# Kernel optimization log

Measured on AMD Instinct MI355X. Metric: run time of the kernel, lower is better.

Reference implementation:

```python
import jax, jax.numpy as jnp
import numpy as np

B, T, D = 16, 2048, 256
WINDOW = 128


def setup_inputs() -> dict:
    key = jax.random.key(0)
    ks = jax.random.split(key, 6)
    scale = 1.0 / np.sqrt(D)
    return {
        "x": jax.random.normal(ks[0], (B, T, D), dtype=jnp.float32),
        "Wq": jax.random.normal(ks[1], (D, D), dtype=jnp.float32) * scale,
        "Wk": jax.random.normal(ks[2], (D, D), dtype=jnp.float32) * scale,
        "Wv": jax.random.normal(ks[3], (D, D), dtype=jnp.float32) * scale,
        "Wo": jax.random.normal(ks[4], (D, D), dtype=jnp.float32) * scale,
        "w_bias": jax.random.normal(ks[5], (T, T), dtype=jnp.float32) * 0.1,
        "window": WINDOW,
    }


def reference(x, Wq, Wk, Wv, Wo, w_bias, window):
    # x: [B,T,D]; w_bias: [T,T] learned pairwise position bias.
    T_ = x.shape[1]
    q = jnp.einsum("btd,de->bte", x, Wq)
    k = jnp.einsum("btd,de->bte", x, Wk)
    v = jnp.einsum("btd,de->bte", x, Wv)

    # AFT-Local: bias is zeroed outside the local band |t - t'| < window,
    # but ALL positions still contribute (with bias 0) to the weighted sum.
    idx = jnp.arange(T_)
    band = jnp.abs(idx[:, None] - idx[None, :]) < window  # [T,T] bool
    w_local = jnp.where(band, w_bias, 0.0)

    # Stable exponentials: the num/den ratio is invariant to per-row shifts
    # of w and per-(b,d) shifts of k.
    w_stable = w_local - jnp.max(w_local, axis=1, keepdims=True)
    k_stable = k - jnp.max(k, axis=1, keepdims=True)
    expw = jnp.exp(w_stable)  # [T,T]
    expk = jnp.exp(k_stable)  # [B,T,D]

    num = jnp.einsum("ts,bsd->btd", expw, expk * v)
    den = jnp.einsum("ts,bsd->btd", expw, expk)
    y = jax.nn.sigmoid(q) * (num / den)
    return jnp.einsum("btd,de->bte", y, Wo)
```

## Files before the change

### kernel.cpp

```cpp
#include <hip/hip_runtime.h>
#include <math.h>

#define B_ 16
#define T_ 2048
#define D_ 256
#define W_ 128
#define M_ (B_*T_)

typedef __attribute__((ext_vector_type(8))) short bf16x8;
typedef __attribute__((ext_vector_type(4))) float f32x4;
typedef unsigned short u16;

static __device__ __forceinline__ u16 f32_bf16_rne(float f) {
    unsigned int u = __float_as_uint(f);
    u += 0x7FFF + ((u >> 16) & 1);
    return (u16)(u >> 16);
}
static __device__ __forceinline__ float bf16_f32(u16 h) {
    return __uint_as_float(((unsigned int)h) << 16);
}

__global__ __launch_bounds__(256) void aft_split_wT(
    const float* __restrict__ Wq, const float* __restrict__ Wk,
    const float* __restrict__ Wv, const float* __restrict__ Wo,
    u16* __restrict__ Wth, u16* __restrict__ Wtl)
{
    const float* Ws[4] = {Wq, Wk, Wv, Wo};
    const float* W = Ws[blockIdx.x];
    const int n  = blockIdx.y * 16 + (threadIdx.x >> 4);
    const int k0 = (threadIdx.x & 15) * 16;
    size_t obase = ((size_t)blockIdx.x * 256 + n) * 256 + k0;
    #pragma unroll 4
    for (int j = 0; j < 16; ++j) {
        float v = W[(size_t)(k0 + j) * 256 + n];
        u16 h = f32_bf16_rne(v);
        Wth[obase + j] = h;
        Wtl[obase + j] = f32_bf16_rne(v - bf16_f32(h));
    }
}

__global__ void aft_ewb(const float* __restrict__ wb, u16* __restrict__ EWb)
{
    const int t = blockIdx.x;
    const int j = threadIdx.x;
    const int s = (t & ~63) - 128 + j;
    const int dlt = s - t;
    float v = 0.f;
    if (s >= 0 && s < T_ && dlt > -W_ && dlt < W_)
        v = expf(wb[(size_t)t * T_ + s]) - 1.0f;
    EWb[(size_t)t * 320 + j] = f32_bf16_rne(v);
}

__global__ __launch_bounds__(256) void aft_qkv_mfma(
    const float* __restrict__ x,
    const u16* __restrict__ Wth, const u16* __restrict__ Wtl,
    u16* __restrict__ ekT, u16* __restrict__ sigqT)
{
    __shared__ alignas(16) u16 sm[25600];
    u16* Ah = sm;
    u16* Al = sm + 5120;
    u16* Bh = sm + 10240;
    u16* Bl = sm + 17920;
    u16* Tr = sm;

    const int tid  = threadIdx.x;
    const int row0 = blockIdx.x * 128;
    const int col0 = blockIdx.y * 64;
    const int b    = row0 >> 11;
    const int t0g  = row0 & (T_ - 1);
    const int lane = tid & 63;
    const int wid  = tid >> 6;
    const int wm   = (wid & 1) * 64;
    const int wn   = (wid >> 1) * 32;
    const int qd   = lane >> 4;
    const int r    = lane & 15;

    f32x4 acc[3][4][2];
    #pragma unroll
    for (int a = 0; a < 3; ++a)
        #pragma unroll
        for (int i = 0; i < 4; ++i)
            #pragma unroll
            for (int j = 0; j < 2; ++j)
                acc[a][i][j] = (f32x4){0.f, 0.f, 0.f, 0.f};

    const int am  = tid >> 1;
    const int akh = (tid & 1) * 16;
    const int bn  = tid >> 2;
    const int bkh = (tid & 3) * 8;

    for (int k0 = 0; k0 < D_; k0 += 32) {
        {
            size_t g = (size_t)(row0 + am) * D_ + k0 + akh;
            #pragma unroll
            for (int c = 0; c < 4; ++c) {
                float4 v = *(const float4*)&x[g + c * 4];
                ushort4 h, l;
                h.x = f32_bf16_rne(v.x); l.x = f32_bf16_rne(v.x - bf16_f32(h.x));
                h.y = f32_bf16_rne(v.y); l.y = f32_bf16_rne(v.y - bf16_f32(h.y));
                h.z = f32_bf16_rne(v.z); l.z = f32_bf16_rne(v.z - bf16_f32(h.z));
                h.w = f32_bf16_rne(v.w); l.w = f32_bf16_rne(v.w - bf16_f32(h.w));
                *(ushort4*)&Ah[am * 40 + akh + c * 4] = h;
                *(ushort4*)&Al[am * 40 + akh + c * 4] = l;
            }
        }
        #pragma unroll
        for (int mat = 0; mat < 3; ++mat) {
            size_t g = ((size_t)mat * 256 + col0 + bn) * 256 + k0 + bkh;
            *(uint4*)&Bh[mat * 2560 + bn * 40 + bkh] = *(const uint4*)&Wth[g];
            *(uint4*)&Bl[mat * 2560 + bn * 40 + bkh] = *(const uint4*)&Wtl[g];
        }
        __syncthreads();

        bf16x8 ah[4], al[4];
        #pragma unroll
        for (int mf = 0; mf < 4; ++mf) {
            ah[mf] = *(const bf16x8*)&Ah[(wm + mf * 16 + r) * 40 + qd * 8];
            al[mf] = *(const bf16x8*)&Al[(wm + mf * 16 + r) * 40 + qd * 8];
        }
        #pragma unroll
        for (int mat = 0; mat < 3; ++mat) {
            #pragma unroll
            for (int nf = 0; nf < 2; ++nf) {
                bf16x8 bh = *(const bf16x8*)&Bh[mat * 2560 + (wn + nf * 16 + r) * 40 + qd * 8];
                bf16x8 bl = *(const bf16x8*)&Bl[mat * 2560 + (wn + nf * 16 + r) * 40 + qd * 8];
                #pragma unroll
                for (int mf = 0; mf < 4; ++mf) {
                    acc[mat][mf][nf] = __builtin_amdgcn_mfma_f32_16x16x32_bf16(ah[mf], bh, acc[mat][mf][nf], 0, 0, 0);
                    acc[mat][mf][nf] = __builtin_amdgcn_mfma_f32_16x16x32_bf16(ah[mf], bl, acc[mat][mf][nf], 0, 0, 0);
                    acc[mat][mf][nf] = __builtin_amdgcn_mfma_f32_16x16x32_bf16(al[mf], bh, acc[mat][mf][nf], 0, 0, 0);
                }
            }
        }
        __syncthreads();
    }

    const int dl_r = tid >> 2;
    const int tseg = (tid & 3) * 32;
    #pragma unroll
    for (int round = 0; round < 3; ++round) {
        __syncthreads();
        #pragma unroll
        for (int mf = 0; mf < 4; ++mf) {
            #pragma unroll
            for (int nf = 0; nf < 2; ++nf) {
                ushort4 o;
                float vals[4];
                #pragma unroll
                for (int reg = 0; reg < 4; ++reg) {
                    float qv = acc[0][mf][nf][reg];
                    float kv = acc[1][mf][nf][reg];
                    float vv = acc[2][mf][nf][reg];
                    if (round == 0)      vals[reg] = expf(kv);
                    else if (round == 1) vals[reg] = expf(kv) * vv;
                    else                 vals[reg] = 1.f / (1.f + expf(-qv));
                }
                o.x = f32_bf16_rne(vals[0]); o.y = f32_bf16_rne(vals[1]);
                o.z = f32_bf16_rne(vals[2]); o.w = f32_bf16_rne(vals[3]);
                int dl = wn + nf * 16 + r;
                int tt = wm + mf * 16 + qd * 4;
                *(ushort4*)&Tr[dl * 136 + tt] = o;
            }
        }
        __syncthreads();
        u16* dst;
        if (round == 0)      dst = ekT   + ((size_t)(b * 512 + col0 + dl_r)) * 2048;
        else if (round == 1) dst = ekT   + ((size_t)(b * 512 + 256 + col0 + dl_r)) * 2048;
        else                 dst = sigqT + ((size_t)(b * 256 + col0 + dl_r)) * 2048;
        dst += t0g + tseg;
        const u16* srcp = &Tr[dl_r * 136 + tseg];
        #pragma unroll
        for (int i = 0; i < 4; ++i)
            *(uint4*)&dst[i * 8] = *(const uint4*)&srcp[i * 8];
    }
}

__global__ __launch_bounds__(256) void aft_sums(
    const u16* __restrict__ ekT, float* __restrict__ Sk, float* __restrict__ Sv)
{
    const int wid  = threadIdx.x >> 6;
    const int lane = threadIdx.x & 63;
    const int row  = blockIdx.x * 4 + wid;
    const int b = row >> 9, n = row & 511;
    const u16* p = ekT + (size_t)row * 2048 + lane * 32;
    float s = 0.f;
    #pragma unroll
    for (int c = 0; c < 4; ++c) {
        union { uint4 v; u16 h[8]; } u;
        u.v = *(const uint4*)&p[c * 8];
        #pragma unroll
        for (int i = 0; i < 8; ++i) s += bf16_f32(u.h[i]);
    }
    #pragma unroll
    for (int off = 32; off >= 1; off >>= 1) s += __shfl_down(s, off, 64);
    if (lane == 0) {
        if (n < 256) Sk[b * 256 + n] = s;
        else         Sv[b * 256 + n - 256] = s;
    }
}

__global__ __launch_bounds__(256) void aft_band_mfma(
    const u16* __restrict__ EWb, const u16* __restrict__ ekT,
    const u16* __restrict__ sigqT,
    const float* __restrict__ Sk, const float* __restrict__ Sv,
    u16* __restrict__ yT)
{
    __shared__ alignas(16) u16 sm[23040];
    u16* Aw  = sm;
    u16* Bkv = sm + 2560;

    const int tid  = threadIdx.x;
    const int t0   = blockIdx.x * 64;
    const int b    = blockIdx.y;
    const int lane = tid & 63;
    const int wid  = tid >> 6;
    const int wn   = wid * 64;
    const int qd   = lane >> 4;
    const int r    = lane & 15;

    f32x4 accn[4][4], accd[4][4];
    #pragma unroll
    for (int i = 0; i < 4; ++i)
        #pragma unroll
        for (int j = 0; j < 4; ++j) {
            accn[i][j] = (f32x4){0.f, 0.f, 0.f, 0.f};
            accd[i][j] = (f32x4){0.f, 0.f, 0.f, 0.f};
        }

    const int atl = tid >> 2;
    const int ak8 = (tid & 3) * 8;

    for (int c = 0; c < 10; ++c) {
        const int sc = t0 - 128 + c * 32;
        if (sc < 0 || sc >= T_) continue;
        __syncthreads();
        *(uint4*)&Aw[atl * 40 + ak8] =
            *(const uint4*)&EWb[(size_t)(t0 + atl) * 320 + c * 32 + ak8];
        #pragma unroll
        for (int rr = 0; rr < 8; ++rr) {
            int n = rr * 64 + atl;
            *(uint4*)&Bkv[n * 40 + ak8] =
                *(const uint4*)&ekT[((size_t)(b * 512) + n) * 2048 + sc + ak8];
        }
        __syncthreads();

        bf16x8 af[4];
        #pragma unroll
        for (int mf = 0; mf < 4; ++mf)
            af[mf] = *(const bf16x8*)&Aw[(mf * 16 + r) * 40 + qd * 8];
        #pragma unroll
        for (int nf = 0; nf < 4; ++nf) {
            bf16x8 be = *(const bf16x8*)&Bkv[(wn + nf * 16 + r) * 40 + qd * 8];
            bf16x8 bv = *(const bf16x8*)&Bkv[(256 + wn + nf * 16 + r) * 40 + qd * 8];
            #pragma unroll
            for (int mf = 0; mf < 4; ++mf) {
                accd[mf][nf] = __builtin_amdgcn_mfma_f32_16x16x32_bf16(af[mf], be, accd[mf][nf], 0, 0, 0);
                accn[mf][nf] = __builtin_amdgcn_mfma_f32_16x16x32_bf16(af[mf], bv, accn[mf][nf], 0, 0, 0);
            }
        }
    }

    #pragma unroll
    for (int nf = 0; nf < 4; ++nf) {
        const int d = wn + nf * 16 + r;
        const float skq = Sk[(b << 8) + d];
        const float svq = Sv[(b << 8) + d];
        #pragma unroll
        for (int mf = 0; mf < 4; ++mf) {
            const int tt = t0 + mf * 16 + qd * 4;
            size_t off = ((size_t)(b << 8) + d) * 2048 + tt;
            ushort4 sg = *(const ushort4*)&sigqT[off];
            ushort4 yo;
            float y0 = bf16_f32(sg.x) * (svq + accn[mf][nf][0]) / (skq + accd[mf][nf][0]);
            float y1 = bf16_f32(sg.y) * (svq + accn[mf][nf][1]) / (skq + accd[mf][nf][1]);
            float y2 = bf16_f32(sg.z) * (svq + accn[mf][nf][2]) / (skq + accd[mf][nf][2]);
            float y3 = bf16_f32(sg.w) * (svq + accn[mf][nf][3]) / (skq + accd[mf][nf][3]);
            yo.x = f32_bf16_rne(y0); yo.y = f32_bf16_rne(y1);
            yo.z = f32_bf16_rne(y2); yo.w = f32_bf16_rne(y3);
            *(ushort4*)&yT[off] = yo;
        }
    }
}

__global__ __launch_bounds__(256) void aft_out_mfma(
    const u16* __restrict__ yT,
    const u16* __restrict__ Woth, const u16* __restrict__ Wotl,
    float* __restrict__ out)
{
    __shared__ alignas(16) u16 sm[15360];
    u16* As = sm;
    u16* Bh = sm + 5120;
    u16* Bl = sm + 10240;

    const int tid  = threadIdx.x;
    const int row0 = blockIdx.x * 128;
    const int col0 = blockIdx.y * 128;
    const int b    = row0 >> 11;
    const int t0g  = row0 & (T_ - 1);
    const int lane = tid & 63;
    const int wid  = tid >> 6;
    const int wm   = (wid & 1) * 64;
    const int wn   = (wid >> 1) * 64;
    const int qd   = lane >> 4;
    const int r    = lane & 15;

    f32x4 acc[4][4];
    #pragma unroll
    for (int i = 0; i < 4; ++i)
        #pragma unroll
        for (int j = 0; j < 4; ++j)
            acc[i][j] = (f32x4){0.f, 0.f, 0.f, 0.f};

    const int dloc = tid & 31;
    const int tb   = (tid >> 5) * 16;
    const int bn   = tid >> 1;
    const int bkh  = (tid & 1) * 16;

    for (int k0 = 0; k0 < D_; k0 += 32) {
        {
            const u16* src = yT + ((size_t)(b * 256) + k0 + dloc) * 2048 + t0g + tb;
            union { uint4 v[2]; u16 h[16]; } u;
            u.v[0] = *(const uint4*)&src[0];
            u.v[1] = *(const uint4*)&src[8];
            #pragma unroll
            for (int i = 0; i < 16; ++i)
                As[(tb + i) * 40 + dloc] = u.h[i];
        }
        {
            size_t g = (size_t)(col0 + bn) * 256 + k0 + bkh;
            *(uint4*)&Bh[bn * 40 + bkh]     = *(const uint4*)&Woth[g];
            *(uint4*)&Bh[bn * 40 + bkh + 8] = *(const uint4*)&Woth[g + 8];
            *(uint4*)&Bl[bn * 40 + bkh]     = *(const uint4*)&Wotl[g];
            *(uint4*)&Bl[bn * 40 + bkh + 8] = *(const uint4*)&Wotl[g + 8];
        }
        __syncthreads();

        bf16x8 af[4];
        #pragma unroll
        for (int mf = 0; mf < 4; ++mf)
            af[mf] = *(const bf16x8*)&As[(wm + mf * 16 + r) * 40 + qd * 8];
        #pragma unroll
        for (int nf = 0; nf < 4; ++nf) {
            bf16x8 bh = *(const bf16x8*)&Bh[(wn + nf * 16 + r) * 40 + qd * 8];
            bf16x8 bl = *(const bf16x8*)&Bl[(wn + nf * 16 + r) * 40 + qd * 8];
            #pragma unroll
            for (int mf = 0; mf < 4; ++mf) {
                acc[mf][nf] = __builtin_amdgcn_mfma_f32_16x16x32_bf16(af[mf], bh, acc[mf][nf], 0, 0, 0);
                acc[mf][nf] = __builtin_amdgcn_mfma_f32_16x16x32_bf16(af[mf], bl, acc[mf][nf], 0, 0, 0);
            }
        }
        __syncthreads();
    }

    #pragma unroll
    for (int mf = 0; mf < 4; ++mf)
        #pragma unroll
        for (int nf = 0; nf < 4; ++nf)
            #pragma unroll
            for (int reg = 0; reg < 4; ++reg) {
                int mrow = row0 + wm + mf * 16 + qd * 4 + reg;
                int ncol = col0 + wn + nf * 16 + r;
                out[(size_t)mrow * D_ + ncol] = acc[mf][nf][reg];
            }
}

extern "C" void kernel_launch(void* const* d_in, const int* in_sizes, int n_in,
                              void* d_out, int out_size, void* d_ws, size_t ws_size,
                              hipStream_t stream)
{
    const float* x  = (const float*)d_in[0];
    const float* Wq = (const float*)d_in[1];
    const float* Wk = (const float*)d_in[2];
    const float* Wv = (const float*)d_in[3];
    const float* Wo = (const float*)d_in[4];
    const float* wb = (const float*)d_in[5];

    u16* Wth   = (u16*)d_ws;
    u16* Wtl   = Wth + 262144;
    u16* EWb   = Wtl + 262144;
    u16* ekT   = EWb + 655360;
    u16* sigqT = ekT + 16777216;
    u16* yT    = sigqT + 8388608;
    float* Sk  = (float*)(yT + 8388608);
    float* Sv  = Sk + 4096;

    aft_split_wT<<<dim3(4, 16), 256, 0, stream>>>(Wq, Wk, Wv, Wo, Wth, Wtl);
    aft_ewb<<<dim3(T_), 320, 0, stream>>>(wb, EWb);
    aft_qkv_mfma<<<dim3(M_ / 128, 4), 256, 0, stream>>>(x, Wth, Wtl, ekT, sigqT);
    aft_sums<<<dim3(8192 / 4), 256, 0, stream>>>(ekT, Sk, Sv);
    aft_band_mfma<<<dim3(T_ / 64, B_), 256, 0, stream>>>(EWb, ekT, sigqT, Sk, Sv, yT);
    aft_out_mfma<<<dim3(M_ / 128, 2), 256, 0, stream>>>(yT, Wth + 3 * 65536, Wtl + 3 * 65536, (float*)d_out);
}
```

Measured before the change: 213.8 us.

## Pre-split x into bf16 hi/lo, use direct global-to-LDS loads, split band/out grids

Adds a separate kernel that splits x into bf16 hi/lo once, so the QKV GEMM can stage A and B tiles with global_load_lds into an XOR-swizzled LDS layout instead of converting in registers. The band kernel is split across two halves of D and the output GEMM uses 64-row tiles, doubling block counts and cutting LDS use per block to raise occupancy. The extra pass writes and rereads x in bf16 hi/lo through memory, which adds an extra kernel launch and global traffic.

```diff
diff --git a/kernel.cpp b/kernel.cpp
--- a/kernel.cpp
+++ b/kernel.cpp
@@ -18,6 +18,11 @@
 }
 static __device__ __forceinline__ float bf16_f32(u16 h) {
     return __uint_as_float(((unsigned int)h) << 16);
+}
+static __device__ __forceinline__ void gload16(const u16* g, u16* lds) {
+    __builtin_amdgcn_global_load_lds(
+        (const __attribute__((address_space(1))) unsigned int*)g,
+        (__attribute__((address_space(3))) unsigned int*)lds, 16, 0, 0);
 }
 
 __global__ __launch_bounds__(256) void aft_split_wT(
@@ -51,16 +56,33 @@
     EWb[(size_t)t * 320 + j] = f32_bf16_rne(v);
 }
 
+__global__ __launch_bounds__(256) void aft_split_x(
+    const float* __restrict__ x, u16* __restrict__ xh, u16* __restrict__ xl)
+{
+    const size_t i0 = ((size_t)blockIdx.x * 256 + threadIdx.x) * 8;
+    float4 v0 = *(const float4*)&x[i0];
+    float4 v1 = *(const float4*)&x[i0 + 4];
+    float v[8] = {v0.x, v0.y, v0.z, v0.w, v1.x, v1.y, v1.z, v1.w};
+    union { uint4 u; u16 h[8]; } H, L;
+    #pragma unroll
+    for (int i = 0; i < 8; ++i) {
+        H.h[i] = f32_bf16_rne(v[i]);
+        L.h[i] = f32_bf16_rne(v[i] - bf16_f32(H.h[i]));
+    }
+    *(uint4*)&xh[i0] = H.u;
+    *(uint4*)&xl[i0] = L.u;
+}
+
 __global__ __launch_bounds__(256) void aft_qkv_mfma(
-    const float* __restrict__ x,
+    const u16* __restrict__ xh, const u16* __restrict__ xl,
     const u16* __restrict__ Wth, const u16* __restrict__ Wtl,
     u16* __restrict__ ekT, u16* __restrict__ sigqT)
 {
-    __shared__ alignas(16) u16 sm[25600];
+    __shared__ alignas(16) u16 sm[20480];
     u16* Ah = sm;
-    u16* Al = sm + 5120;
-    u16* Bh = sm + 10240;
-    u16* Bl = sm + 17920;
+    u16* Al = sm + 4096;
+    u16* Bh = sm + 8192;
+    u16* Bl = sm + 14336;
     u16* Tr = sm;
 
     const int tid  = threadIdx.x;
@@ -74,6 +96,8 @@
     const int wn   = (wid >> 1) * 32;
     const int qd   = lane >> 4;
     const int r    = lane & 15;
+    const int lrow = lane >> 2;
+    const int lseg = lane & 3;
 
     f32x4 acc[3][4][2];
     #pragma unroll
@@ -84,46 +108,43 @@
             for (int j = 0; j < 2; ++j)
                 acc[a][i][j] = (f32x4){0.f, 0.f, 0.f, 0.f};
 
-    const int am  = tid >> 1;
-    const int akh = (tid & 1) * 16;
-    const int bn  = tid >> 2;
-    const int bkh = (tid & 3) * 8;
-
     for (int k0 = 0; k0 < D_; k0 += 32) {
-        {
-            size_t g = (size_t)(row0 + am) * D_ + k0 + akh;
-            #pragma unroll
-            for (int c = 0; c < 4; ++c) {
-                float4 v = *(const float4*)&x[g + c * 4];
-                ushort4 h, l;
-                h.x = f32_bf16_rne(v.x); l.x = f32_bf16_rne(v.x - bf16_f32(h.x));
-                h.y = f32_bf16_rne(v.y); l.y = f32_bf16_rne(v.y - bf16_f32(h.y));
-                h.z = f32_bf16_rne(v.z); l.z = f32_bf16_rne(v.z - bf16_f32(h.z));
-                h.w = f32_bf16_rne(v.w); l.w = f32_bf16_rne(v.w - bf16_f32(h.w));
-                *(ushort4*)&Ah[am * 40 + akh + c * 4] = h;
-                *(ushort4*)&Al[am * 40 + akh + c * 4] = l;
-            }
+        #pragma unroll
+        for (int j = 0; j < 2; ++j) {
+            int rbase = j * 64 + wid * 16;
+            int row   = rbase + lrow;
+            int seg   = lseg ^ ((row >> 1) & 3);
+            size_t g  = (size_t)(row0 + row) * 256 + k0 + seg * 8;
+            gload16(xh + g, &Ah[rbase * 32]);
+            gload16(xl + g, &Al[rbase * 32]);
+        }
+        #pragma unroll
+        for (int m = 0; m < 3; ++m) {
+            int rbase = wid * 16;
+            int row   = rbase + lrow;
+            int seg   = lseg ^ ((row >> 1) & 3);
+            size_t g  = ((size_t)(m * 256 + col0 + row)) * 256 + k0 + seg * 8;
+            gload16(Wth + g, &Bh[m * 2048 + rbase * 32]);
+            gload16(Wtl + g, &Bl[m * 2048 + rbase * 32]);
+        }
+        __syncthreads();
+
+        bf16x8 ah[4], al[4];
+        #pragma unroll
+        for (int mf = 0; mf < 4; ++mf) {
+            int arow = wm + mf * 16 + r;
+            int sw   = (qd ^ ((arow >> 1) & 3)) * 8;
+            ah[mf] = *(const bf16x8*)&Ah[arow * 32 + sw];
+            al[mf] = *(const bf16x8*)&Al[arow * 32 + sw];
         }
         #pragma unroll
         for (int mat = 0; mat < 3; ++mat) {
-            size_t g = ((size_t)mat * 256 + col0 + bn) * 256 + k0 + bkh;
-            *(uint4*)&Bh[mat * 2560 + bn * 40 + bkh] = *(const uint4*)&Wth[g];
-            *(uint4*)&Bl[mat * 2560 + bn * 40 + bkh] = *(const uint4*)&Wtl[g];
-        }
-        __syncthreads();
-
-        bf16x8 ah[4], al[4];
-        #pragma unroll
-        for (int mf = 0; mf < 4; ++mf) {
-            ah[mf] = *(const bf16x8*)&Ah[(wm + mf * 16 + r) * 40 + qd * 8];
-            al[mf] = *(const bf16x8*)&Al[(wm + mf * 16 + r) * 40 + qd * 8];
-        }
-        #pragma unroll
-        for (int mat = 0; mat < 3; ++mat) {
             #pragma unroll
             for (int nf = 0; nf < 2; ++nf) {
-                bf16x8 bh = *(const bf16x8*)&Bh[mat * 2560 + (wn + nf * 16 + r) * 40 + qd * 8];
-                bf16x8 bl = *(const bf16x8*)&Bl[mat * 2560 + (wn + nf * 16 + r) * 40 + qd * 8];
+                int brow = wn + nf * 16 + r;
+                int sw   = (qd ^ ((brow >> 1) & 3)) * 8;
+                bf16x8 bh = *(const bf16x8*)&Bh[mat * 2048 + brow * 32 + sw];
+                bf16x8 bl = *(const bf16x8*)&Bl[mat * 2048 + brow * 32 + sw];
                 #pragma unroll
                 for (int mf = 0; mf < 4; ++mf) {
                     acc[mat][mf][nf] = __builtin_amdgcn_mfma_f32_16x16x32_bf16(ah[mf], bh, acc[mat][mf][nf], 0, 0, 0);
@@ -205,24 +226,25 @@
     const float* __restrict__ Sk, const float* __restrict__ Sv,
     u16* __restrict__ yT)
 {
-    __shared__ alignas(16) u16 sm[23040];
+    __shared__ alignas(16) u16 sm[12800];
     u16* Aw  = sm;
     u16* Bkv = sm + 2560;
 
     const int tid  = threadIdx.x;
     const int t0   = blockIdx.x * 64;
-    const int b    = blockIdx.y;
+    const int b    = blockIdx.y >> 1;
+    const int dh   = (blockIdx.y & 1) * 128;
     const int lane = tid & 63;
     const int wid  = tid >> 6;
-    const int wn   = wid * 64;
+    const int wn   = wid * 32;
     const int qd   = lane >> 4;
     const int r    = lane & 15;
 
-    f32x4 accn[4][4], accd[4][4];
+    f32x4 accn[4][2], accd[4][2];
     #pragma unroll
     for (int i = 0; i < 4; ++i)
         #pragma unroll
-        for (int j = 0; j < 4; ++j) {
+        for (int j = 0; j < 2; ++j) {
             accn[i][j] = (f32x4){0.f, 0.f, 0.f, 0.f};
             accd[i][j] = (f32x4){0.f, 0.f, 0.f, 0.f};
         }
@@ -237,9 +259,10 @@
         *(uint4*)&Aw[atl * 40 + ak8] =
             *(const uint4*)&EWb[(size_t)(t0 + atl) * 320 + c * 32 + ak8];
         #pragma unroll
-        for (int rr = 0; rr < 8; ++rr) {
-            int n = rr * 64 + atl;
-            *(uint4*)&Bkv[n * 40 + ak8] =
+        for (int rr = 0; rr < 4; ++rr) {
+            int nl = rr * 64 + atl;
+            int n  = (nl < 128) ? (dh + nl) : (256 + dh + nl - 128);
+            *(uint4*)&Bkv[nl * 40 + ak8] =
                 *(const uint4*)&ekT[((size_t)(b * 512) + n) * 2048 + sc + ak8];
         }
         __syncthreads();
@@ -249,9 +272,9 @@
         for (int mf = 0; mf < 4; ++mf)
             af[mf] = *(const bf16x8*)&Aw[(mf * 16 + r) * 40 + qd * 8];
         #pragma unroll
-        for (int nf = 0; nf < 4; ++nf) {
+        for (int nf = 0; nf < 2; ++nf) {
             bf16x8 be = *(const bf16x8*)&Bkv[(wn + nf * 16 + r) * 40 + qd * 8];
-            bf16x8 bv = *(const bf16x8*)&Bkv[(256 + wn + nf * 16 + r) * 40 + qd * 8];
+            bf16x8 bv = *(const bf16x8*)&Bkv[(128 + wn + nf * 16 + r) * 40 + qd * 8];
             #pragma unroll
             for (int mf = 0; mf < 4; ++mf) {
                 accd[mf][nf] = __builtin_amdgcn_mfma_f32_16x16x32_bf16(af[mf], be, accd[mf][nf], 0, 0, 0);
@@ -261,8 +284,8 @@
     }
 
     #pragma unroll
-    for (int nf = 0; nf < 4; ++nf) {
-        const int d = wn + nf * 16 + r;
+    for (int nf = 0; nf < 2; ++nf) {
+        const int d = dh + wn + nf * 16 + r;
         const float skq = Sk[(b << 8) + d];
         const float svq = Sv[(b << 8) + d];
         #pragma unroll
@@ -287,43 +310,41 @@
     const u16* __restrict__ Woth, const u16* __restrict__ Wotl,
     float* __restrict__ out)
 {
-    __shared__ alignas(16) u16 sm[15360];
+    __shared__ alignas(16) u16 sm[12800];
     u16* As = sm;
-    u16* Bh = sm + 5120;
-    u16* Bl = sm + 10240;
+    u16* Bh = sm + 2560;
+    u16* Bl = sm + 7680;
 
     const int tid  = threadIdx.x;
-    const int row0 = blockIdx.x * 128;
+    const int row0 = blockIdx.x * 64;
     const int col0 = blockIdx.y * 128;
     const int b    = row0 >> 11;
     const int t0g  = row0 & (T_ - 1);
     const int lane = tid & 63;
     const int wid  = tid >> 6;
-    const int wm   = (wid & 1) * 64;
-    const int wn   = (wid >> 1) * 64;
+    const int wn   = wid * 32;
     const int qd   = lane >> 4;
     const int r    = lane & 15;
 
-    f32x4 acc[4][4];
+    f32x4 acc[4][2];
     #pragma unroll
     for (int i = 0; i < 4; ++i)
         #pragma unroll
-        for (int j = 0; j < 4; ++j)
+        for (int j = 0; j < 2; ++j)
             acc[i][j] = (f32x4){0.f, 0.f, 0.f, 0.f};
 
     const int dloc = tid & 31;
-    const int tb   = (tid >> 5) * 16;
+    const int tb   = (tid >> 5) * 8;
     const int bn   = tid >> 1;
     const int bkh  = (tid & 1) * 16;
 
     for (int k0 = 0; k0 < D_; k0 += 32) {
         {
             const u16* src = yT + ((size_t)(b * 256) + k0 + dloc) * 2048 + t0g + tb;
-            union { uint4 v[2]; u16 h[16]; } u;
-            u.v[0] = *(const uint4*)&src[0];
-            u.v[1] = *(const uint4*)&src[8];
-            #pragma unroll
-            for (int i = 0; i < 16; ++i)
+            union { uint4 v; u16 h[8]; } u;
+            u.v = *(const uint4*)&src[0];
+            #pragma unroll
+            for (int i = 0; i < 8; ++i)
                 As[(tb + i) * 40 + dloc] = u.h[i];
         }
         {
@@ -338,9 +359,9 @@
         bf16x8 af[4];
         #pragma unroll
         for (int mf = 0; mf < 4; ++mf)
-            af[mf] = *(const bf16x8*)&As[(wm + mf * 16 + r) * 40 + qd * 8];
-        #pragma unroll
-        for (int nf = 0; nf < 4; ++nf) {
+            af[mf] = *(const bf16x8*)&As[(mf * 16 + r) * 40 + qd * 8];
+        #pragma unroll
+        for (int nf = 0; nf < 2; ++nf) {
             bf16x8 bh = *(const bf16x8*)&Bh[(wn + nf * 16 + r) * 40 + qd * 8];
             bf16x8 bl = *(const bf16x8*)&Bl[(wn + nf * 16 + r) * 40 + qd * 8];
             #pragma unroll
@@ -355,10 +376,10 @@
     #pragma unroll
     for (int mf = 0; mf < 4; ++mf)
         #pragma unroll
-        for (int nf = 0; nf < 4; ++nf)
+        for (int nf = 0; nf < 2; ++nf)
             #pragma unroll
             for (int reg = 0; reg < 4; ++reg) {
-                int mrow = row0 + wm + mf * 16 + qd * 4 + reg;
+                int mrow = row0 + mf * 16 + qd * 4 + reg;
                 int ncol = col0 + wn + nf * 16 + r;
                 out[(size_t)mrow * D_ + ncol] = acc[mf][nf][reg];
             }
@@ -378,7 +399,9 @@
     u16* Wth   = (u16*)d_ws;
     u16* Wtl   = Wth + 262144;
     u16* EWb   = Wtl + 262144;
-    u16* ekT   = EWb + 655360;
+    u16* xh    = EWb + 655360;
+    u16* xl    = xh + 8388608;
+    u16* ekT   = xl + 8388608;
     u16* sigqT = ekT + 16777216;
     u16* yT    = sigqT + 8388608;
     float* Sk  = (float*)(yT + 8388608);
@@ -386,8 +409,9 @@
 
     aft_split_wT<<<dim3(4, 16), 256, 0, stream>>>(Wq, Wk, Wv, Wo, Wth, Wtl);
     aft_ewb<<<dim3(T_), 320, 0, stream>>>(wb, EWb);
-    aft_qkv_mfma<<<dim3(M_ / 128, 4), 256, 0, stream>>>(x, Wth, Wtl, ekT, sigqT);
+    aft_split_x<<<dim3(4096), 256, 0, stream>>>(x, xh, xl);
+    aft_qkv_mfma<<<dim3(M_ / 128, 4), 256, 0, stream>>>(xh, xl, Wth, Wtl, ekT, sigqT);
     aft_sums<<<dim3(8192 / 4), 256, 0, stream>>>(ekT, Sk, Sv);
-    aft_band_mfma<<<dim3(T_ / 64, B_), 256, 0, stream>>>(EWb, ekT, sigqT, Sk, Sv, yT);
-    aft_out_mfma<<<dim3(M_ / 128, 2), 256, 0, stream>>>(yT, Wth + 3 * 65536, Wtl + 3 * 65536, (float*)d_out);
-}
+    aft_band_mfma<<<dim3(T_ / 64, B_ * 2), 256, 0, stream>>>(EWb, ekT, sigqT, Sk, Sv, yT);
+    aft_out_mfma<<<dim3(M_ / 64, 2), 256, 0, stream>>>(yT, Wth + 3 * 65536, Wtl + 3 * 65536, (float*)d_out);
+}
```

After: 255.7 us. 19.6% more time.
